# Performance work log

Hardware: AMD Instinct MI355X
Metric: run time of the kernel (lower is better)

## Reference

```python
import jax, jax.numpy as jnp
import numpy as np

SCALE = 20.0
TEMP = 1.0
POW = 0.5
SINK_TAU = 0.3
SINK_ITERS = 30
LAMBDA_LC = 1.0
EPS = 1e-12


def _l2norm(f):
    # F.normalize(f, p=2, dim=channel) * 20 ; f: [B,N,C], normalize over C
    n = jnp.sqrt(jnp.sum(f * f, axis=-1, keepdims=True))
    return f / jnp.maximum(n, EPS) * SCALE


def _sinkhorn(log_alpha, n_iters):
    # log-space Sinkhorn normalization (gumbel_sinkhorn with n_samples=1, no noise)
    def body(la, _):
        la = la - jax.nn.logsumexp(la, axis=2, keepdims=True)  # row normalize
        la = la - jax.nn.logsumexp(la, axis=1, keepdims=True)  # col normalize
        return la, None
    la, _ = jax.lax.scan(body, log_alpha, None, length=n_iters)
    return jnp.exp(la)


def setup_inputs() -> dict:
    key = jax.random.key(0)
    k1, k2 = jax.random.split(key)
    feats = jax.random.normal(k1, (16, 1024, 128), dtype=jnp.float32)
    pc0 = jax.random.normal(k2, (8, 1024, 3), dtype=jnp.float32)
    return {"feats": feats, "pc0": pc0, "epoch": 0}


def reference(feats, pc0, epoch):
    B, N, _ = pc0.shape
    f1 = _l2norm(feats[0::2])                 # [B,N,C]
    f2 = _l2norm(feats[1::2])                 # [B,N,C]
    fa = jnp.roll(f1, -1, axis=0)             # anchor feats1[(b+1)%B]

    corr_1a = jnp.einsum('bnc,bmc->bnm', f1, fa) / TEMP
    smcorr_1a = jax.nn.softmax(corr_1a, axis=2)
    f1_via_fa = jnp.einsum('bnm,bmc->bnc', smcorr_1a, fa)
    corr_1a2 = jnp.einsum('bnc,bmc->bnm', f1_via_fa, f2) / TEMP
    smcorr_1a2 = jax.nn.softmax(corr_1a2, axis=2)

    # Sinkhorn branch is under torch.no_grad()
    sink = jax.lax.stop_gradient(_sinkhorn(corr_1a2 / SINK_TAU, SINK_ITERS))

    # pairwise distance weights (no_grad)
    diff = pc0[:, :, None, :] - pc0[:, None, :, :]            # [B,N,N,3]
    dist = jax.lax.stop_gradient(jnp.sqrt(jnp.sum(diff * diff, axis=-1)) ** POW)

    corr_12 = jnp.einsum('bnc,bmc->bnm', f1, f2)
    smcorr_12 = jax.nn.softmax(corr_12 / TEMP, axis=2)

    L = dist * (smcorr_1a2 + smcorr_12)                       # L = dist*sm1a2 + dist*sm12
    loss = jnp.sum(L) / N                                     # sum over b of L.sum()/N

    eye = jnp.eye(N, dtype=sink.dtype)
    perm_to_I = 3.0 * jnp.sum(jnp.abs(eye[None] - sink)) / N
    Lc = 3.0 * jnp.sum(jnp.abs(sink - smcorr_1a2)) / N

    correct_match = jnp.sum(
        (jnp.argmax(smcorr_1a2, axis=2) == jnp.arange(N)[None, :]).astype(jnp.float32)
    )

    total_loss = loss + LAMBDA_LC * Lc
    Bf = jnp.float32(B)
    return (total_loss / Bf, loss / Bf, Lc / Bf, correct_match / Bf, perm_to_I / Bf)
```

## Files before the change

kernel.cpp:

```cpp
#include <hip/hip_runtime.h>
#include <math.h>

#define NB 8
#define NN 1024
#define NC 128
#define INV_TAU (1.0f/0.3f)
#define LOG2E 1.44269504088896340736f

typedef unsigned short u16;
typedef short bf16x8 __attribute__((ext_vector_type(8)));
typedef float f32x4 __attribute__((ext_vector_type(4)));

__device__ __forceinline__ float wsum(float v){
  #pragma unroll
  for (int o = 32; o > 0; o >>= 1) v += __shfl_xor(v, o, 64);
  return v;
}
__device__ __forceinline__ float wmax(float v){
  #pragma unroll
  for (int o = 32; o > 0; o >>= 1) v = fmaxf(v, __shfl_xor(v, o, 64));
  return v;
}
__device__ __forceinline__ float fexp2(float x){ return __builtin_amdgcn_exp2f(x); }
__device__ __forceinline__ float flog2(float x){ return __builtin_amdgcn_logf(x); }
__device__ __forceinline__ u16 f2bf(float f){
  unsigned u = __float_as_uint(f);
  return (u16)((u + 0x7FFFu + ((u >> 16) & 1u)) >> 16);
}
__device__ __forceinline__ float bf2f(u16 h){ return __uint_as_float((unsigned)h << 16); }

__device__ __forceinline__ void load16(const float* __restrict__ base, int lane, float* o){
  float4 a = *(const float4*)(base + 8 * lane);
  float4 b = *(const float4*)(base + 8 * lane + 4);
  float4 c = *(const float4*)(base + 512 + 8 * lane);
  float4 d = *(const float4*)(base + 512 + 8 * lane + 4);
  o[0]=a.x; o[1]=a.y; o[2]=a.z; o[3]=a.w; o[4]=b.x; o[5]=b.y; o[6]=b.z; o[7]=b.w;
  o[8]=c.x; o[9]=c.y; o[10]=c.z; o[11]=c.w; o[12]=d.x; o[13]=d.y; o[14]=d.z; o[15]=d.w;
}

__global__ void k_init(float* accs, float* P, float* V){
  int i = blockIdx.x * 256 + threadIdx.x;
  if (i < 160) accs[i] = 0.0f;
  P[i] = 0.0f; V[i] = 0.0f;
}

__global__ void k_normalize(const float* __restrict__ feats, float* __restrict__ f1,
                            u16* __restrict__ f1h, u16* __restrict__ f1l,
                            u16* __restrict__ f2h, u16* __restrict__ f2l){
  int vid = blockIdx.x;
  int lane = threadIdx.x;
  const float* src = feats + (size_t)vid * NC;
  float2 x = *(const float2*)(src + lane * 2);
  float s = wsum(x.x * x.x + x.y * x.y);
  float sc = 20.0f / fmaxf(sqrtf(s), 1e-12f);
  int batch = vid >> 10, n = vid & 1023;
  size_t off = ((size_t)(batch >> 1) * NN + n) * NC + 2 * lane;
  float2 y; y.x = x.x * sc; y.y = x.y * sc;
  u16 h0 = f2bf(y.x), h1 = f2bf(y.y);
  u16 l0 = f2bf(y.x - bf2f(h0)), l1 = f2bf(y.y - bf2f(h1));
  unsigned hw = (unsigned)h0 | ((unsigned)h1 << 16);
  unsigned lw = (unsigned)l0 | ((unsigned)l1 << 16);
  if (batch & 1){
    *(unsigned*)(f2h + off) = hw; *(unsigned*)(f2l + off) = lw;
  } else {
    *(float2*)(f1 + off) = y;
    *(unsigned*)(f1h + off) = hw; *(unsigned*)(f1l + off) = lw;
  }
}

__global__ __launch_bounds__(256) void k_transp(const u16* __restrict__ H,
                                                const u16* __restrict__ L,
                                                u16* __restrict__ TH, u16* __restrict__ TL){
  __shared__ u16 T[64][72];
  int b = blockIdx.z, n0 = blockIdx.y * 64, c0 = blockIdx.x * 64;
  int tid = threadIdx.x;
  #pragma unroll
  for (int pass = 0; pass < 2; pass++){
    const u16* src = (pass ? L : H) + (size_t)b * NN * NC;
    u16* dst = (pass ? TL : TH) + (size_t)b * NC * NN;
    #pragma unroll
    for (int i = 0; i < 2; i++){
      int unit = tid + 256 * i;
      int r = unit >> 3, u = unit & 7;
      *(uint4*)&T[r][u * 8] = *(const uint4*)(src + (size_t)(n0 + r) * NC + c0 + u * 8);
    }
    __syncthreads();
    #pragma unroll
    for (int i = 0; i < 2; i++){
      int unit = tid + 256 * i;
      int c = unit >> 3, nu = unit & 7;
      u16 vals[8];
      #pragma unroll
      for (int k = 0; k < 8; k++) vals[k] = T[nu * 8 + k][c];
      *(uint4*)(dst + (size_t)(c0 + c) * NN + n0 + nu * 8) = *(uint4*)vals;
    }
    __syncthreads();
  }
}

__global__ __launch_bounds__(256) void k_gemm_mfma(const u16* __restrict__ Ah_g,
                                                   const u16* __restrict__ Al_g,
                                                   const u16* __restrict__ Bh_g,
                                                   const u16* __restrict__ Bl_g,
                                                   void* __restrict__ Cm,
                                                   int rollB, int q16){
  __shared__ __align__(16) u16 As_h[128][64];
  __shared__ __align__(16) u16 As_l[128][64];
  __shared__ __align__(16) u16 Bs_h[128][64];
  __shared__ __align__(16) u16 Bs_l[128][64];
  const float QS12 = 32766.0f / 400.0f;
  int b = blockIdx.z;
  int m0 = blockIdx.x * 128, n0 = blockIdx.y * 128;
  int tid = threadIdx.x, w = tid >> 6, lane = tid & 63;
  int quad = lane >> 4, l15 = lane & 15;
  int wn = (w >> 1) * 64, wm = (w & 1) * 64;
  size_t abase = (size_t)b * NN * NC;
  size_t bbase = (size_t)((b + rollB) & 7) * NN * NC;
  f32x4 z = {0.0f, 0.0f, 0.0f, 0.0f};
  f32x4 acc[4][4] = {{z,z,z,z},{z,z,z,z},{z,z,z,z},{z,z,z,z}};
  for (int kk = 0; kk < NC; kk += 64){
    #pragma unroll
    for (int i2 = 0; i2 < 4; i2++){
      int uidx = tid + 256 * i2;
      int r = uidx >> 3, u = uidx & 7;
      int su = ((u ^ (r & 7)) << 3);
      size_t goA = abase + (size_t)(n0 + r) * NC + kk + u * 8;
      size_t goB = bbase + (size_t)(m0 + r) * NC + kk + u * 8;
      *(uint4*)&As_h[r][su] = *(const uint4*)(Ah_g + goA);
      *(uint4*)&As_l[r][su] = *(const uint4*)(Al_g + goA);
      *(uint4*)&Bs_h[r][su] = *(const uint4*)(Bh_g + goB);
      *(uint4*)&Bs_l[r][su] = *(const uint4*)(Bl_g + goB);
    }
    __syncthreads();
    #pragma unroll
    for (int c = 0; c < 2; c++){
      bf16x8 ah[4], al[4], bh[4], bl[4];
      #pragma unroll
      for (int i = 0; i < 4; i++){
        int rn = wn + i * 16 + l15;
        int sn = (((c * 4 + quad) ^ (rn & 7)) << 3);
        ah[i] = *(const bf16x8*)&As_h[rn][sn];
        al[i] = *(const bf16x8*)&As_l[rn][sn];
        int rm = wm + i * 16 + l15;
        int sm = (((c * 4 + quad) ^ (rm & 7)) << 3);
        bh[i] = *(const bf16x8*)&Bs_h[rm][sm];
        bl[i] = *(const bf16x8*)&Bs_l[rm][sm];
      }
      #pragma unroll
      for (int i = 0; i < 4; i++)
        #pragma unroll
        for (int j = 0; j < 4; j++){
          acc[i][j] = __builtin_amdgcn_mfma_f32_16x16x32_bf16(ah[i], bh[j], acc[i][j], 0, 0, 0);
          acc[i][j] = __builtin_amdgcn_mfma_f32_16x16x32_bf16(ah[i], bl[j], acc[i][j], 0, 0, 0);
          acc[i][j] = __builtin_amdgcn_mfma_f32_16x16x32_bf16(al[i], bh[j], acc[i][j], 0, 0, 0);
        }
    }
    __syncthreads();
  }
  if (q16){
    short* Cb = (short*)Cm + (size_t)b * NN * NN;
    #pragma unroll
    for (int i = 0; i < 4; i++)
      #pragma unroll
      for (int j = 0; j < 4; j++)
        #pragma unroll
        for (int r = 0; r < 4; r++){
          int n = n0 + wn + i * 16 + quad * 4 + r;
          int m = m0 + wm + j * 16 + l15;
          float q = rintf(fminf(fmaxf(acc[i][j][r] * QS12, -32766.0f), 32766.0f));
          Cb[(size_t)n * NN + m] = (short)(int)q;
        }
  } else {
    float* Cb = (float*)Cm + (size_t)b * NN * NN;
    #pragma unroll
    for (int i = 0; i < 4; i++)
      #pragma unroll
      for (int j = 0; j < 4; j++)
        #pragma unroll
        for (int r = 0; r < 4; r++){
          int n = n0 + wn + i * 16 + quad * 4 + r;
          int m = m0 + wm + j * 16 + l15;
          Cb[(size_t)n * NN + m] = acc[i][j][r];
        }
  }
}

__global__ void k_rowstats(const float* __restrict__ Mb, float* __restrict__ lse){
  int row = blockIdx.x * 4 + (threadIdx.x >> 6);
  int lane = threadIdx.x & 63;
  const float* p = Mb + (size_t)row * NN;
  float x[16]; float mx = -3.402823466e38f;
  #pragma unroll
  for (int k = 0; k < 16; k++){ x[k] = p[lane + 64 * k]; mx = fmaxf(mx, x[k]); }
  mx = wmax(mx);
  float s = 0.0f;
  #pragma unroll
  for (int k = 0; k < 16; k++) s += expf(x[k] - mx);
  s = wsum(s);
  if (lane == 0) lse[row] = mx + logf(s);
}

__global__ void k_rowstats_argmax(const float* __restrict__ Mb, float* __restrict__ lse,
                                  float* __restrict__ accs){
  __shared__ float axs[4];
  int row = blockIdx.x * 4 + (threadIdx.x >> 6);
  int wid = threadIdx.x >> 6;
  int lane = threadIdx.x & 63;
  const float* p = Mb + (size_t)row * NN;
  float x[16]; float mx = -3.402823466e38f; float ax = 0.0f;
  float bm = -3.402823466e38f; int bi = 0;
  #pragma unroll
  for (int k = 0; k < 16; k++){
    x[k] = p[lane + 64 * k];
    mx = fmaxf(mx, x[k]);
    ax = fmaxf(ax, fabsf(x[k]));
    if (x[k] > bm){ bm = x[k]; bi = lane + 64 * k; }
  }
  mx = wmax(mx); ax = wmax(ax);
  #pragma unroll
  for (int o = 32; o > 0; o >>= 1){
    float om = __shfl_xor(bm, o, 64); int oi = __shfl_xor(bi, o, 64);
    if (om > bm || (om == bm && oi < bi)){ bm = om; bi = oi; }
  }
  float s = 0.0f;
  #pragma unroll
  for (int k = 0; k < 16; k++) s += expf(x[k] - mx);
  s = wsum(s);
  if (lane == 0){
    lse[row] = mx + logf(s);
    axs[wid] = ax;
    if (bi == (row & 1023)) atomicAdd(&accs[48 + (blockIdx.x & 15)], 1.0f);
  }
  __syncthreads();
  if (threadIdx.x == 0){
    float a = fmaxf(fmaxf(axs[0], axs[1]), fmaxf(axs[2], axs[3]));
    atomicMax((int*)&accs[64 + (blockIdx.x & 15)], __float_as_int(a));
  }
}

__global__ void k_scale(float* accs){
  if (threadIdx.x == 0){
    float g = 0.0f;
    for (int j = 0; j < 16; j++) g = fmaxf(g, accs[64 + j]);
    accs[80] = (g * INV_TAU * LOG2E) / 32766.0f;
  }
}

__global__ __launch_bounds__(256) void k_fva_mfma(const float* __restrict__ Mg,
                                                  const float* __restrict__ lse1,
                                                  const u16* __restrict__ f1Th,
                                                  const u16* __restrict__ f1Tl,
                                                  float* __restrict__ fva){
  __shared__ __align__(16) u16 Ph[128][64];
  __shared__ __align__(16) u16 Pl[128][64];
  __shared__ __align__(16) u16 Fh[128][64];
  __shared__ __align__(16) u16 Fl[128][64];
  int b = blockIdx.z, zq = blockIdx.x, ny = blockIdx.y;
  int n0 = ny * 128, mbase = zq * 256;
  const float* Mb = Mg + ((size_t)(b * NN + n0)) * NN + mbase;
  const u16* fTh = f1Th + (size_t)((b + 1) & 7) * NC * NN;
  const u16* fTl = f1Tl + (size_t)((b + 1) & 7) * NC * NN;
  const float* lseb = lse1 + b * NN + n0;
  float* out = fva + (size_t)zq * 1048576 + ((size_t)(b * NN + n0)) * NC;
  int tid = threadIdx.x, w = tid >> 6, lane = tid & 63;
  int quad = lane >> 4, l15 = lane & 15;
  int wn = (w >> 1) * 64, wc = (w & 1) * 64;
  f32x4 z = {0.0f, 0.0f, 0.0f, 0.0f};
  f32x4 acc[4][4] = {{z,z,z,z},{z,z,z,z},{z,z,z,z},{z,z,z,z}};
  for (int mm = 0; mm < 256; mm += 64){
    #pragma unroll
    for (int i2 = 0; i2 < 4; i2++){
      int unit = tid + 256 * i2;
      int r = unit >> 3, u = unit & 7;
      int su = ((u ^ (r & 7)) << 3);
      float l = lseb[r];
      const float* mp = Mb + (size_t)r * NN + mm + u * 8;
      float4 v0 = *(const float4*)mp, v1 = *(const float4*)(mp + 4);
      float p[8] = { fexp2((v0.x - l) * LOG2E), fexp2((v0.y - l) * LOG2E),
                     fexp2((v0.z - l) * LOG2E), fexp2((v0.w - l) * LOG2E),
                     fexp2((v1.x - l) * LOG2E), fexp2((v1.y - l) * LOG2E),
                     fexp2((v1.z - l) * LOG2E), fexp2((v1.w - l) * LOG2E) };
      u16 h[8], lo[8];
      #pragma unroll
      for (int k = 0; k < 8; k++){ h[k] = f2bf(p[k]); lo[k] = f2bf(p[k] - bf2f(h[k])); }
      uint4 hw, lw;
      hw.x = (unsigned)h[0] | ((unsigned)h[1] << 16);  hw.y = (unsigned)h[2] | ((unsigned)h[3] << 16);
      hw.z = (unsigned)h[4] | ((unsigned)h[5] << 16);  hw.w = (unsigned)h[6] | ((unsigned)h[7] << 16);
      lw.x = (unsigned)lo[0] | ((unsigned)lo[1] << 16); lw.y = (unsigned)lo[2] | ((unsigned)lo[3] << 16);
      lw.z = (unsigned)lo[4] | ((unsigned)lo[5] << 16); lw.w = (unsigned)lo[6] | ((unsigned)lo[7] << 16);
      *(uint4*)&Ph[r][su] = hw;
      *(uint4*)&Pl[r][su] = lw;
      size_t fo = (size_t)r * NN + mbase + mm + u * 8;
      *(uint4*)&Fh[r][su] = *(const uint4*)(fTh + fo);
      *(uint4*)&Fl[r][su] = *(const uint4*)(fTl + fo);
    }
    __syncthreads();
    #pragma unroll
    for (int c2 = 0; c2 < 2; c2++){
      bf16x8 ph[4], pl[4], fh[4], fl[4];
      #pragma unroll
      for (int i = 0; i < 4; i++){
        int rn = wn + i * 16 + l15;
        int sn = (((c2 * 4 + quad) ^ (rn & 7)) << 3);
        ph[i] = *(const bf16x8*)&Ph[rn][sn];
        pl[i] = *(const bf16x8*)&Pl[rn][sn];
        int rc = wc + i * 16 + l15;
        int sc = (((c2 * 4 + quad) ^ (rc & 7)) << 3);
        fh[i] = *(const bf16x8*)&Fh[rc][sc];
        fl[i] = *(const bf16x8*)&Fl[rc][sc];
      }
      #pragma unroll
      for (int i = 0; i < 4; i++)
        #pragma unroll
        for (int j = 0; j < 4; j++){
          acc[i][j] = __builtin_amdgcn_mfma_f32_16x16x32_bf16(ph[i], fh[j], acc[i][j], 0, 0, 0);
          acc[i][j] = __builtin_amdgcn_mfma_f32_16x16x32_bf16(ph[i], fl[j], acc[i][j], 0, 0, 0);
          acc[i][j] = __builtin_amdgcn_mfma_f32_16x16x32_bf16(pl[i], fh[j], acc[i][j], 0, 0, 0);
        }
    }
    __syncthreads();
  }
  #pragma unroll
  for (int i = 0; i < 4; i++)
    #pragma unroll
    for (int j = 0; j < 4; j++)
      #pragma unroll
      for (int r = 0; r < 4; r++){
        int n = wn + i * 16 + quad * 4 + r;
        int c = wc + j * 16 + l15;
        out[(size_t)n * NC + c] = acc[i][j][r];
      }
}

__global__ __launch_bounds__(256) void k_split(const float* __restrict__ A,
                                               u16* __restrict__ H, u16* __restrict__ L){
  int g = blockIdx.x * 256 + threadIdx.x;
  float4 a = ((const float4*)A)[g];
  float4 b = ((const float4*)(A + 1048576))[g];
  float4 c = ((const float4*)(A + 2097152))[g];
  float4 d = ((const float4*)(A + 3145728))[g];
  float s[4] = { a.x + b.x + c.x + d.x, a.y + b.y + c.y + d.y,
                 a.z + b.z + c.z + d.z, a.w + b.w + c.w + d.w };
  u16 h[4], l[4];
  #pragma unroll
  for (int k = 0; k < 4; k++){
    h[k] = f2bf(s[k]);
    l[k] = f2bf(s[k] - bf2f(h[k]));
  }
  uint2 hw, lw;
  hw.x = (unsigned)h[0] | ((unsigned)h[1] << 16); hw.y = (unsigned)h[2] | ((unsigned)h[3] << 16);
  lw.x = (unsigned)l[0] | ((unsigned)l[1] << 16); lw.y = (unsigned)l[2] | ((unsigned)l[3] << 16);
  ((uint2*)H)[g] = hw; ((uint2*)L)[g] = lw;
}

__global__ __launch_bounds__(256) void k_quant_t(const float* __restrict__ Mb,
                                                 const float* __restrict__ accs,
                                                 short* __restrict__ Q,
                                                 short* __restrict__ Qt){
  __shared__ float T[64][68];
  float KQ = (INV_TAU * LOG2E) / accs[80];
  int b = blockIdx.z; int n0 = blockIdx.y * 64, m0 = blockIdx.x * 64;
  const float* src = Mb + (size_t)b * NN * NN;
  int tid = threadIdx.x;
  #pragma unroll
  for (int i = 0; i < 4; i++){
    int t = tid + 256 * i; int r = t >> 4, c4 = t & 15;
    float4 v = *(const float4*)(src + (size_t)(n0 + r) * NN + m0 + c4 * 4);
    float q0 = rintf(v.x * KQ);
    float q1 = rintf(v.y * KQ);
    float q2 = rintf(v.z * KQ);
    float q3 = rintf(v.w * KQ);
    T[r][c4*4+0] = q0; T[r][c4*4+1] = q1; T[r][c4*4+2] = q2; T[r][c4*4+3] = q3;
    int2 w;
    w.x = ((int)q0 & 0xFFFF) | ((int)q1 << 16);
    w.y = ((int)q2 & 0xFFFF) | ((int)q3 << 16);
    *(int2*)(Q + ((size_t)(b * NN + n0 + r) * NN + m0 + c4 * 4)) = w;
  }
  __syncthreads();
  #pragma unroll
  for (int i = 0; i < 4; i++){
    int t = tid + 256 * i; int r = t >> 4, c4 = t & 15;
    float q0 = T[c4*4+0][r], q1 = T[c4*4+1][r], q2 = T[c4*4+2][r], q3 = T[c4*4+3][r];
    int2 w;
    w.x = ((int)q0 & 0xFFFF) | ((int)q1 << 16);
    w.y = ((int)q2 & 0xFFFF) | ((int)q3 << 16);
    *(int2*)(Qt + ((size_t)(b * NN + m0 + r) * NN + n0 + c4 * 4)) = w;
  }
}

__global__ __launch_bounds__(1024) void k_pass(const short* __restrict__ Q,
                                               const float* __restrict__ invec,
                                               float* __restrict__ outvec,
                                               const float* __restrict__ accs){
  const float IQ2 = accs[80];
  int tid = threadIdx.x, wid = tid >> 6, lane = tid & 63;
  int row = blockIdx.x * 16 + wid;
  int b = row >> 10;
  float hh[16];
  load16(invec + b * NN, lane, hh);
  const int4* qp = (const int4*)(Q + (size_t)row * NN);
  int4 wa = qp[lane], wb = qp[64 + lane];
  int qq[8] = { wa.x, wa.y, wa.z, wa.w, wb.x, wb.y, wb.z, wb.w };
  float x[16]; float mx = -3.402823466e38f;
  #pragma unroll
  for (int k = 0; k < 8; k++){
    x[2*k]   = fmaf((float)(short)(qq[k]), IQ2, hh[2*k]);
    x[2*k+1] = fmaf((float)(qq[k] >> 16),  IQ2, hh[2*k+1]);
    mx = fmaxf(mx, fmaxf(x[2*k], x[2*k+1]));
  }
  mx = wmax(mx);
  float s = 0.0f;
  #pragma unroll
  for (int k = 0; k < 16; k++) s += fexp2(x[k] - mx);
  s = wsum(s);
  if (lane == 0) outvec[row] = -(mx + flog2(s));
}

__global__ __launch_bounds__(1024) void k_final(const short* __restrict__ Q,
                                                const short* __restrict__ Q12,
                                                const float* __restrict__ lse2,
                                                const float* __restrict__ P2,
                                                const float* __restrict__ V2,
                                                const float* __restrict__ pc0,
                                                float* __restrict__ accs){
  __shared__ float pcx[1152], pcy[1152], pcz[1152];
  __shared__ float partial[3][16];
  const float IQ2 = accs[80];
  const float IQ12_2 = (400.0f / 32766.0f) * LOG2E;
  int tid = threadIdx.x, wid = tid >> 6, lane = tid & 63;
  int row = blockIdx.x * 16 + wid;
  int b = row >> 10, n = row & 1023;
  {
    int m = tid;
    const float* pg = pc0 + (size_t)b * 3072 + 3 * m;
    float px = pg[0], py = pg[1], pz = pg[2];
    int idx = m + (m >> 3);
    pcx[idx] = px; pcy[idx] = py; pcz[idx] = pz;
  }
  __syncthreads();
  const int4* qp  = (const int4*)(Q   + (size_t)row * NN);
  const int4* qp2 = (const int4*)(Q12 + (size_t)row * NN);
  int4 a1 = qp[lane],  b1 = qp[64 + lane];
  int4 a2 = qp2[lane], b2 = qp2[64 + lane];
  int q1[8] = { a1.x, a1.y, a1.z, a1.w, b1.x, b1.y, b1.z, b1.w };
  int q2[8] = { a2.x, a2.y, a2.z, a2.w, b2.x, b2.y, b2.z, b2.w };
  float L[16], c[16];
  float cmx = -3.402823466e38f;
  #pragma unroll
  for (int k = 0; k < 8; k++){
    L[2*k]   = (float)(short)(q1[k]) * IQ2;
    L[2*k+1] = (float)(q1[k] >> 16)  * IQ2;
    c[2*k]   = (float)(short)(q2[k]) * IQ12_2;
    c[2*k+1] = (float)(q2[k] >> 16)  * IQ12_2;
    cmx = fmaxf(cmx, fmaxf(c[2*k], c[2*k+1]));
  }
  cmx = wmax(cmx);
  float cs = 0.0f;
  #pragma unroll
  for (int k = 0; k < 16; k++) cs += fexp2(c[k] - cmx);
  cs = wsum(cs);
  float lse12r = cmx + flog2(cs);
  float vv[16];
  load16(V2 + b * NN, lane, vv);
  int nidx = n + (n >> 3);
  float qx = pcx[nidx], qy = pcy[nidx], qz = pcz[nidx];
  float c1row = -lse2[row] * LOG2E;
  float Prow = P2[row];
  float sl = 0.0f, slc = 0.0f, spi = 0.0f;
  #pragma unroll
  for (int k = 0; k < 16; k++){
    int m = (k < 8) ? (8 * lane + k) : (512 + 8 * lane + k - 8);
    int midx = m + (m >> 3);
    float e1 = fexp2(fmaf(L[k], 0.3f, c1row));
    float sk = fexp2(L[k] + Prow + vv[k]);
    float e2 = fexp2(c[k] - lse12r);
    float dx = qx - pcx[midx], dy = qy - pcy[midx], dz = qz - pcz[midx];
    float d = sqrtf(sqrtf(dx*dx + dy*dy + dz*dz));
    sl  += d * (e1 + e2);
    slc += fabsf(sk - e1);
    spi += fabsf(((m == n) ? 1.0f : 0.0f) - sk);
  }
  sl = wsum(sl); slc = wsum(slc); spi = wsum(spi);
  if (lane == 0){ partial[0][wid] = sl; partial[1][wid] = slc; partial[2][wid] = spi; }
  __syncthreads();
  if (tid < 3){
    float t = 0.0f;
    #pragma unroll
    for (int i = 0; i < 16; i++) t += partial[tid][i];
    atomicAdd(&accs[tid * 16 + (blockIdx.x & 15)], t);
  }
}

__global__ void k_finalize(const float* __restrict__ accs, float* __restrict__ out){
  if (threadIdx.x == 0){
    float sl = 0, slc = 0, spi = 0, scm = 0;
    for (int j = 0; j < 16; j++){
      sl += accs[j]; slc += accs[16 + j]; spi += accs[32 + j]; scm += accs[48 + j];
    }
    float loss = sl / 1024.0f;
    float Lc   = 3.0f * slc / 1024.0f;
    float perm = 3.0f * spi / 1024.0f;
    float total = loss + Lc;
    out[0] = total / 8.0f;
    out[1] = loss / 8.0f;
    out[2] = Lc / 8.0f;
    out[3] = scm / 8.0f;
    out[4] = perm / 8.0f;
  }
}

extern "C" void kernel_launch(void* const* d_in, const int* in_sizes, int n_in,
                              void* d_out, int out_size, void* d_ws, size_t ws_size,
                              hipStream_t stream){
  const float* feats = (const float*)d_in[0];
  const float* pc0   = (const float*)d_in[1];
  float* out = (float*)d_out;

  float* ws   = (float*)d_ws;
  float* f1   = ws;
  u16* f1h    = (u16*)(f1 + 1048576);
  u16* f1l    = f1h + 1048576;
  u16* f2h    = f1l + 1048576;
  u16* f2l    = f2h + 1048576;
  u16* f1Th   = f2l + 1048576;
  u16* f1Tl   = f1Th + 1048576;
  u16* fvh    = f1Tl + 1048576;
  u16* fvl    = fvh + 1048576;
  float* fva  = (float*)(fvl + 1048576);
  float* M    = fva + 4194304;
  short* Q    = (short*)(M + 8388608);
  short* Qt   = Q + 8388608;
  float* lse1 = (float*)(Qt + 8388608);
  float* lse2 = lse1 + 8192;
  float* P    = lse2 + 8192;
  float* V    = P + 8192;
  float* accs = V + 8192;
  if (ws_size < (size_t)((char*)(accs + 160) - (char*)ws)) return;

  k_init<<<32, 256, 0, stream>>>(accs, P, V);
  k_normalize<<<16384, 64, 0, stream>>>(feats, f1, f1h, f1l, f2h, f2l);
  k_transp<<<dim3(2,16,8), 256, 0, stream>>>(f1h, f1l, f1Th, f1Tl);
  k_gemm_mfma<<<dim3(8,8,8), 256, 0, stream>>>(f1h, f1l, f1h, f1l, M, 1, 0);
  k_rowstats<<<2048, 256, 0, stream>>>(M, lse1);
  k_fva_mfma<<<dim3(4,8,8), 256, 0, stream>>>(M, lse1, f1Th, f1Tl, fva);
  k_split<<<1024, 256, 0, stream>>>(fva, fvh, fvl);
  k_gemm_mfma<<<dim3(8,8,8), 256, 0, stream>>>(fvh, fvl, f2h, f2l, M, 0, 0);
  k_rowstats_argmax<<<2048, 256, 0, stream>>>(M, lse2, accs);
  k_scale<<<1, 64, 0, stream>>>(accs);
  k_quant_t<<<dim3(16,16,8), 256, 0, stream>>>(M, accs, Q, Qt);
  for (int it = 0; it < 30; it++){
    k_pass<<<512, 1024, 0, stream>>>(Q,  V, P, accs);
    k_pass<<<512, 1024, 0, stream>>>(Qt, P, V, accs);
  }
  k_gemm_mfma<<<dim3(8,8,8), 256, 0, stream>>>(f1h, f1l, f2h, f2l, Qt, 0, 1);
  k_final<<<512, 1024, 0, stream>>>(Q, Qt, lse2, P, V, pc0, accs);
  k_finalize<<<1, 64, 0, stream>>>(accs, out);
}
```

Measured before the change: 461.4 us.

## Fuse Sinkhorn iterations into one cooperative persistent kernel with grid barriers

Replaces the 60 separate row/column logsumexp pass launches with a single cooperative kernel of 256 blocks. Each block keeps its quantized Q and Qt rows in registers across all iterations and synchronizes through an atomic-counter grid barrier. This removes per-launch overhead and the repeated reloading of Q from memory. In exchange, the barrier spin-waits on global atomics and only 256 blocks are active, which lowers parallelism per pass. The counter at accs+128 must be zeroed beforehand, which k_init appears to handle.

```diff
diff --git a/kernel.cpp b/kernel.cpp
--- a/kernel.cpp
+++ b/kernel.cpp
@@ -29,13 +29,22 @@
 }
 __device__ __forceinline__ float bf2f(u16 h){ return __uint_as_float((unsigned)h << 16); }
 
-__device__ __forceinline__ void load16(const float* __restrict__ base, int lane, float* o){
+__device__ __forceinline__ void load16(const float* base, int lane, float* o){
   float4 a = *(const float4*)(base + 8 * lane);
   float4 b = *(const float4*)(base + 8 * lane + 4);
   float4 c = *(const float4*)(base + 512 + 8 * lane);
   float4 d = *(const float4*)(base + 512 + 8 * lane + 4);
   o[0]=a.x; o[1]=a.y; o[2]=a.z; o[3]=a.w; o[4]=b.x; o[5]=b.y; o[6]=b.z; o[7]=b.w;
   o[8]=c.x; o[9]=c.y; o[10]=c.z; o[11]=c.w; o[12]=d.x; o[13]=d.y; o[14]=d.z; o[15]=d.w;
+}
+
+__device__ __forceinline__ void gbar(unsigned* cnt, unsigned target){
+  __syncthreads();
+  if (threadIdx.x == 0){
+    __hip_atomic_fetch_add(cnt, 1u, __ATOMIC_ACQ_REL, __HIP_MEMORY_SCOPE_AGENT);
+    while (__hip_atomic_load(cnt, __ATOMIC_ACQUIRE, __HIP_MEMORY_SCOPE_AGENT) < target){}
+  }
+  __syncthreads();
 }
 
 __global__ void k_init(float* accs, float* P, float* V){
@@ -388,32 +397,71 @@
   }
 }
 
-__global__ __launch_bounds__(1024) void k_pass(const short* __restrict__ Q,
-                                               const float* __restrict__ invec,
-                                               float* __restrict__ outvec,
-                                               const float* __restrict__ accs){
+__global__ __launch_bounds__(1024) void k_sinkhorn(const short* Q, const short* Qt,
+                                                   float* P, float* V, float* accs){
   const float IQ2 = accs[80];
+  unsigned* cnt = (unsigned*)(accs + 128);
   int tid = threadIdx.x, wid = tid >> 6, lane = tid & 63;
-  int row = blockIdx.x * 16 + wid;
-  int b = row >> 10;
-  float hh[16];
-  load16(invec + b * NN, lane, hh);
-  const int4* qp = (const int4*)(Q + (size_t)row * NN);
-  int4 wa = qp[lane], wb = qp[64 + lane];
-  int qq[8] = { wa.x, wa.y, wa.z, wa.w, wb.x, wb.y, wb.z, wb.w };
-  float x[16]; float mx = -3.402823466e38f;
-  #pragma unroll
-  for (int k = 0; k < 8; k++){
-    x[2*k]   = fmaf((float)(short)(qq[k]), IQ2, hh[2*k]);
-    x[2*k+1] = fmaf((float)(qq[k] >> 16),  IQ2, hh[2*k+1]);
-    mx = fmaxf(mx, fmaxf(x[2*k], x[2*k+1]));
-  }
-  mx = wmax(mx);
-  float s = 0.0f;
-  #pragma unroll
-  for (int k = 0; k < 16; k++) s += fexp2(x[k] - mx);
-  s = wsum(s);
-  if (lane == 0) outvec[row] = -(mx + flog2(s));
+  int blk = blockIdx.x;
+  int b = blk >> 5;
+  int row0 = blk * 32 + wid * 2;
+  int4 qa[2], qb[2], ta[2], tb[2];
+  #pragma unroll
+  for (int r = 0; r < 2; r++){
+    const int4* qp = (const int4*)(Q + (size_t)(row0 + r) * NN);
+    qa[r] = qp[lane]; qb[r] = qp[64 + lane];
+    const int4* tp = (const int4*)(Qt + (size_t)(row0 + r) * NN);
+    ta[r] = tp[lane]; tb[r] = tp[64 + lane];
+  }
+  const float* Vb = V + b * NN;
+  const float* Pb = P + b * NN;
+  unsigned target = 0;
+  for (int it = 0; it < 30; it++){
+    {
+      float hh[16];
+      load16(Vb, lane, hh);
+      #pragma unroll
+      for (int r = 0; r < 2; r++){
+        int qq[8] = { qa[r].x, qa[r].y, qa[r].z, qa[r].w, qb[r].x, qb[r].y, qb[r].z, qb[r].w };
+        float x[16]; float mx = -3.402823466e38f;
+        #pragma unroll
+        for (int k = 0; k < 8; k++){
+          x[2*k]   = fmaf((float)(short)(qq[k]), IQ2, hh[2*k]);
+          x[2*k+1] = fmaf((float)(qq[k] >> 16),  IQ2, hh[2*k+1]);
+          mx = fmaxf(mx, fmaxf(x[2*k], x[2*k+1]));
+        }
+        mx = wmax(mx);
+        float s = 0.0f;
+        #pragma unroll
+        for (int k = 0; k < 16; k++) s += fexp2(x[k] - mx);
+        s = wsum(s);
+        if (lane == 0) P[row0 + r] = -(mx + flog2(s));
+      }
+    }
+    target += 256; gbar(cnt, target);
+    {
+      float pp[16];
+      load16(Pb, lane, pp);
+      #pragma unroll
+      for (int r = 0; r < 2; r++){
+        int qq[8] = { ta[r].x, ta[r].y, ta[r].z, ta[r].w, tb[r].x, tb[r].y, tb[r].z, tb[r].w };
+        float x[16]; float mx = -3.402823466e38f;
+        #pragma unroll
+        for (int k = 0; k < 8; k++){
+          x[2*k]   = fmaf((float)(short)(qq[k]), IQ2, pp[2*k]);
+          x[2*k+1] = fmaf((float)(qq[k] >> 16),  IQ2, pp[2*k+1]);
+          mx = fmaxf(mx, fmaxf(x[2*k], x[2*k+1]));
+        }
+        mx = wmax(mx);
+        float s = 0.0f;
+        #pragma unroll
+        for (int k = 0; k < 16; k++) s += fexp2(x[k] - mx);
+        s = wsum(s);
+        if (lane == 0) V[row0 + r] = -(mx + flog2(s));
+      }
+    }
+    if (it < 29){ target += 256; gbar(cnt, target); }
+  }
 }
 
 __global__ __launch_bounds__(1024) void k_final(const short* __restrict__ Q,
@@ -548,9 +596,10 @@
   k_rowstats_argmax<<<2048, 256, 0, stream>>>(M, lse2, accs);
   k_scale<<<1, 64, 0, stream>>>(accs);
   k_quant_t<<<dim3(16,16,8), 256, 0, stream>>>(M, accs, Q, Qt);
-  for (int it = 0; it < 30; it++){
-    k_pass<<<512, 1024, 0, stream>>>(Q,  V, P, accs);
-    k_pass<<<512, 1024, 0, stream>>>(Qt, P, V, accs);
+  {
+    void* args[] = { (void*)&Q, (void*)&Qt, (void*)&P, (void*)&V, (void*)&accs };
+    hipLaunchCooperativeKernel((const void*)(void*)k_sinkhorn, dim3(256), dim3(1024),
+                               args, 0, stream);
   }
   k_gemm_mfma<<<dim3(8,8,8), 256, 0, stream>>>(f1h, f1l, f2h, f2l, Qt, 0, 1);
   k_final<<<512, 1024, 0, stream>>>(Q, Qt, lse2, P, V, pc0, accs);
```

After: 1.212 ms. 2.63x slower.
